# Optimization experiments

Hardware: AMD Instinct MI355X
Metric: run time of the kernel (lower is better)

The kernel has to match this reference:

```python
import jax, jax.numpy as jnp
import numpy as np

N, E, D, H = 100000, 1250000, 64, 128
EPS = 1e-5


def sage_bn_relu(x, src, dst, W_self, b_self, W_neigh, gamma, beta):
    # mean aggregation over in-neighbors (DGL SAGEConv 'mean')
    n = x.shape[0]
    deg = jax.ops.segment_sum(jnp.ones((src.shape[0],), x.dtype), dst, num_segments=n)
    agg = jax.ops.segment_sum(x[src], dst, num_segments=n)  # [N, d]
    neigh = agg / jnp.maximum(deg, 1.0)[:, None]             # zero in-degree -> 0
    h = x @ W_self + b_self + neigh @ W_neigh                # fc_self + fc_neigh
    # BatchNorm1d (training-mode batch statistics, biased variance)
    mu = h.mean(0)
    var = jnp.mean((h - mu) ** 2, axis=0)
    h = (h - mu) * jax.lax.rsqrt(var + EPS) * gamma + beta
    return jax.nn.relu(h)  # dropout omitted (deterministic eval)


def setup_inputs() -> dict:
    key = jax.random.key(0)
    ks = jax.random.split(key, 32)
    inp = {
        "x": jax.random.normal(ks[0], (N, D), jnp.float32),
        "src": jax.random.randint(ks[1], (E,), 0, N),
        "dst": jax.random.randint(ks[2], (E,), 0, N),
    }
    dims = [(D, H), (H, H), (H, H)]
    k = 3
    for i, (din, dout) in enumerate(dims):
        s = 1.0 / np.sqrt(din)
        inp[f"W_self{i}"] = jax.random.uniform(ks[k], (din, dout), jnp.float32, -s, s); k += 1
        inp[f"b_self{i}"] = jnp.zeros((dout,), jnp.float32)
        inp[f"W_neigh{i}"] = jax.random.uniform(ks[k], (din, dout), jnp.float32, -s, s); k += 1
        inp[f"gamma{i}"] = jnp.ones((dout,), jnp.float32)
        inp[f"beta{i}"] = jnp.zeros((dout,), jnp.float32)
    s = 1.0 / np.sqrt(H)
    inp["Wc"] = jax.random.uniform(ks[k], (H, 2), jnp.float32, -s, s)
    inp["bc"] = jnp.zeros((2,), jnp.float32)
    return inp


def reference(x, src, dst,
              W_self0, b_self0, W_neigh0, gamma0, beta0,
              W_self1, b_self1, W_neigh1, gamma1, beta1,
              W_self2, b_self2, W_neigh2, gamma2, beta2,
              Wc, bc):
    h = sage_bn_relu(x, src, dst, W_self0, b_self0, W_neigh0, gamma0, beta0)
    h = sage_bn_relu(h, src, dst, W_self1, b_self1, W_neigh1, gamma1, beta1)
    h = sage_bn_relu(h, src, dst, W_self2, b_self2, W_neigh2, gamma2, beta2)
    return h @ Wc + bc  # [N, 2]
```

## Files before the change

kernel.cpp:

```cpp
#include <hip/hip_runtime.h>


#define N_NODES 100000
#define N_EDGES 1250000
#define NB 1563
#define BSZ 64
#define CAP 1024
#define BPART 256
#define NREP 8
#define INVN (1.0f / 100000.0f)

typedef short bf16x8 __attribute__((ext_vector_type(8)));
typedef float f32x4 __attribute__((ext_vector_type(4)));
typedef unsigned short u16x8 __attribute__((ext_vector_type(8)));
typedef unsigned short u16x4 __attribute__((ext_vector_type(4)));
typedef unsigned short u16x2 __attribute__((ext_vector_type(2)));

__device__ __forceinline__ float bf2f(unsigned short u) {
  union { unsigned int i; float f; } c; c.i = ((unsigned int)u) << 16; return c.f;
}
__device__ __forceinline__ unsigned short f2bf(float f) {
  union { float f; unsigned int i; } c; c.f = f;
  unsigned int r = (c.i + 0x7FFFu + ((c.i >> 16) & 1u)) >> 16;
  return (unsigned short)r;
}
__device__ __forceinline__ void bn_st(const float* stats, const float* gam,
                                      const float* bet, int c, float& s, float& t) {
  float sum = 0.f, sq = 0.f;
  #pragma unroll
  for (int r = 0; r < NREP; r++) {
    sum += stats[r * 256 + c];
    sq  += stats[r * 256 + 128 + c];
  }
  float mu = sum * INVN;
  float var = sq * INVN - mu * mu;
  s = gam[c] * rsqrtf(var + 1e-5f);
  t = bet[c] - mu * s;
}
__device__ __forceinline__ void gload_lds16(const void* g, void* l) {
  __builtin_amdgcn_global_load_lds(
      (const __attribute__((address_space(1))) unsigned int*)g,
      (__attribute__((address_space(3))) unsigned int*)l, 16, 0, 0);
}

__global__ __launch_bounds__(256) void k_prep(
    const float* __restrict__ x, unsigned short* __restrict__ x16,
    const float* __restrict__ W0s, const float* __restrict__ W0n,
    const float* __restrict__ W1s, const float* __restrict__ W1n,
    const float* __restrict__ W2s, const float* __restrict__ W2n,
    unsigned short* __restrict__ wt, float* __restrict__ stats3,
    const int* __restrict__ dst, int* __restrict__ hist, int E) {
  __shared__ int hh[NB];
  int blk = blockIdx.x, t = threadIdx.x;
  if (blk < 6250) {
    int i = blk * 256 + t;
    float4 v = ((const float4*)x)[i];
    u16x4 o;
    o.x = f2bf(v.x); o.y = f2bf(v.y); o.z = f2bf(v.z); o.w = f2bf(v.w);
    ((u16x4*)x16)[i] = o;
  } else if (blk < 6570) {
    int i = (blk - 6250) * 256 + t;
    if (i < 16384) {
      const float* W = (i < 8192) ? W0s : W0n;
      unsigned short* o = wt + (i < 8192 ? 0 : 8192);
      int j = i & 8191;
      int c = j >> 6, k = j & 63;
      o[j] = f2bf(W[k * 128 + c]);
    } else {
      int j = i - 16384;
      int sel = j >> 14;
      j &= 16383;
      const float* W = (sel == 0) ? W1s : (sel == 1) ? W1n : (sel == 2) ? W2s : W2n;
      unsigned short* o = wt + 16384 + sel * 16384;
      int c = j >> 7, k = j & 127;
      o[j] = f2bf(W[k * 128 + c]);
    }
  } else if (blk == 6570) {
    for (int i = t; i < 3 * NREP * 256; i += 256) stats3[i] = 0.f;
  } else {
    int hb = blk - 6571;
    int chunk = (E + BPART - 1) / BPART;
    int start = hb * chunk;
    int end = min(E, start + chunk);
    for (int b = t; b < NB; b += 256) hh[b] = 0;
    __syncthreads();
    for (int e = start + t; e < end; e += 256) atomicAdd(&hh[dst[e] >> 6], 1);
    __syncthreads();
    for (int b = t; b < NB; b += 256) hist[hb * NB + b] = hh[b];
  }
}

__global__ __launch_bounds__(256) void k_scan(const int* __restrict__ hist,
                                              int* __restrict__ base,
                                              int* __restrict__ gcursor) {
  int bb = blockIdx.x * 256 + threadIdx.x;
  if (bb >= NB) return;
  int run = 0;
  for (int r0 = 0; r0 < BPART; r0 += 16) {
    int v[16];
    #pragma unroll
    for (int u = 0; u < 16; u++) v[u] = hist[(r0 + u) * NB + bb];
    #pragma unroll
    for (int u = 0; u < 16; u++) { base[(r0 + u) * NB + bb] = run; run += v[u]; }
  }
  gcursor[bb] = run;
}

__global__ __launch_bounds__(256) void k_scatter(const int* __restrict__ src,
                                                 const int* __restrict__ dst,
                                                 const int* __restrict__ base,
                                                 unsigned int* __restrict__ part, int E) {
  __shared__ int cur[NB];
  int t = threadIdx.x;
  int chunk = (E + BPART - 1) / BPART;
  int start = blockIdx.x * chunk;
  int end = min(E, start + chunk);
  for (int b = t; b < NB; b += 256) cur[b] = base[blockIdx.x * NB + b];
  __syncthreads();
  for (int e = start + t; e < end; e += 256) {
    int d = dst[e];
    int b = d >> 6;
    int pos = atomicAdd(&cur[b], 1);
    if ((unsigned)pos < (unsigned)CAP)
      part[(size_t)b * CAP + pos] = (unsigned)src[e] | ((unsigned)(d & 63) << 17);
  }
}

template <int DIN, bool BN>
__global__ __launch_bounds__(512, 8) void k_layer(
    const unsigned short* __restrict__ h, const unsigned short* __restrict__ W1t,
    const unsigned short* __restrict__ W2t, const float* __restrict__ bias,
    const unsigned int* __restrict__ part, const int* __restrict__ gcursor,
    unsigned short* __restrict__ C, float* __restrict__ stats, int M,
    const float* __restrict__ statsP, const float* __restrict__ gamP,
    const float* __restrict__ betP) {
  __shared__ unsigned short neighT[64 * DIN];
  __shared__ unsigned eord[CAP];
  __shared__ unsigned short Bs[2][128 * 32];
  __shared__ int cnt[BSZ], offv[BSZ], cur[BSZ];
  __shared__ int stealCtr;
  __shared__ float sBN[128], tBN[128];
  unsigned* eraw = (unsigned*)neighT;
  float* redS = (float*)eord;
  float* redQ = redS + 512;

  constexpr int SWZM = (DIN == 128) ? 15 : 7;
  constexpr int KS = DIN / 32;
  int t = threadIdx.x;
  int lane = t & 63, w = t >> 6;
  int l15 = lane & 15, quad = lane >> 4;
  int bkt = blockIdx.x;
  int node0 = bkt * BSZ;
  int nn = min(BSZ, M - node0);

  if (t < BSZ) cnt[t] = 0;
  if (t == 0) stealCtr = 0;
  if (BN && t < 128) bn_st(statsP, gamP, betP, t, sBN[t], tBN[t]);
  __syncthreads();

  int ec = gcursor[bkt];
  ec = max(0, min(ec, CAP));
  for (int i = t; i < ec; i += 512) {
    unsigned wd = part[(size_t)bkt * CAP + i];
    eraw[i] = wd;
    atomicAdd(&cnt[wd >> 17], 1);
  }
  __syncthreads();
  if (w == 0) {
    int v = cnt[lane];
    int incl = v;
    #pragma unroll
    for (int o = 1; o < 64; o <<= 1) {
      int u = __shfl_up(incl, o);
      if (lane >= o) incl += u;
    }
    offv[lane] = incl - v;
    cur[lane] = incl - v;
  }
  __syncthreads();
  for (int i = t; i < ec; i += 512) {
    unsigned wd = eraw[i];
    int p = atomicAdd(&cur[wd >> 17], 1);
    eord[p] = wd & 0x1FFFF;
  }
  __syncthreads();

  const int G = DIN / 8;
  int li = t & (G - 1);
  float sreg[8], treg[8];
  if (BN) {
    #pragma unroll
    for (int k = 0; k < 8; k++) { sreg[k] = sBN[li * 8 + k]; treg[k] = tBN[li * 8 + k]; }
  }
  for (;;) {
    int nd0 = 0;
    if (li == 0) nd0 = atomicAdd(&stealCtr, 1);
    int nd = __shfl(nd0, 0, G);
    if (nd >= BSZ) break;
    u16x8 o;
    if (nd >= nn) {
      #pragma unroll
      for (int k = 0; k < 8; k++) o[k] = 0;
    } else {
      int s = offv[nd], c = cnt[nd];
      int e = s + c;
      float acc[8] = {0.f, 0.f, 0.f, 0.f, 0.f, 0.f, 0.f, 0.f};
      int j = s;
      for (; j + 2 <= e; j += 2) {
        int sn0 = eord[j], sn1 = eord[j + 1];
        u16x8 v0 = *(const u16x8*)&h[(size_t)sn0 * DIN + li * 8];
        u16x8 v1 = *(const u16x8*)&h[(size_t)sn1 * DIN + li * 8];
        if (BN) {
          #pragma unroll
          for (int k = 0; k < 8; k++)
            acc[k] += fmaxf(fmaf(bf2f(v0[k]), sreg[k], treg[k]), 0.f)
                    + fmaxf(fmaf(bf2f(v1[k]), sreg[k], treg[k]), 0.f);
        } else {
          #pragma unroll
          for (int k = 0; k < 8; k++) acc[k] += bf2f(v0[k]) + bf2f(v1[k]);
        }
      }
      if (j < e) {
        int sn = eord[j];
        u16x8 v = *(const u16x8*)&h[(size_t)sn * DIN + li * 8];
        if (BN) {
          #pragma unroll
          for (int k = 0; k < 8; k++)
            acc[k] += fmaxf(fmaf(bf2f(v[k]), sreg[k], treg[k]), 0.f);
        } else {
          #pragma unroll
          for (int k = 0; k < 8; k++) acc[k] += bf2f(v[k]);
        }
      }
      float inv = 1.0f / fmaxf((float)c, 1.0f);
      #pragma unroll
      for (int k = 0; k < 8; k++) o[k] = f2bf(acc[k] * inv);
    }
    *(u16x8*)&neighT[nd * DIN + ((li * 8) ^ ((nd & SWZM) << 3))] = o;
  }

  const int strip = w >> 1;
  const int ch = w & 1;
  const int row = strip * 16 + l15;
  f32x4 acc4[4];
  #pragma unroll
  for (int ct = 0; ct < 4; ct++) acc4[ct] = (f32x4){0.f, 0.f, 0.f, 0.f};

  auto stageBs = [&](int s, int bi) {
    const unsigned short* Wt = (s < KS) ? W1t : W2t;
    int k0 = ((s < KS) ? s : s - KS) * 32;
    int r = t >> 2, prt = t & 3;
    gload_lds16(&Wt[(size_t)r * DIN + k0 + prt * 8], &Bs[bi][(w * 64) * 8]);
  };
  stageBs(0, 0);
  __syncthreads();

  int cb = 0;
  #pragma unroll
  for (int s = 0; s < 2 * KS; s++) {
    if (s + 1 < 2 * KS) stageBs(s + 1, cb ^ 1);
    bf16x8 af;
    if (s < KS) {
      int k0 = s * 32;
      u16x8 v = *(const u16x8*)&h[(size_t)(node0 + row) * DIN + k0 + quad * 8];
      if (BN) {
        #pragma unroll
        for (int j = 0; j < 8; j++) {
          int c = k0 + quad * 8 + j;
          v[j] = f2bf(fmaxf(fmaf(bf2f(v[j]), sBN[c], tBN[c]), 0.f));
        }
      }
      af = *(bf16x8*)&v;
    } else {
      int cc = (s - KS) * 32 + quad * 8;
      u16x8 v = *(const u16x8*)&neighT[row * DIN + (cc ^ ((row & SWZM) << 3))];
      af = *(bf16x8*)&v;
    }
    #pragma unroll
    for (int ct = 0; ct < 4; ct++) {
      bf16x8 bfr = *(const bf16x8*)&Bs[cb][(ch * 64 + ct * 16 + l15) * 32 + quad * 8];
      acc4[ct] = __builtin_amdgcn_mfma_f32_16x16x32_bf16(af, bfr, acc4[ct], 0, 0, 0);
    }
    if (s + 1 < 2 * KS) __syncthreads();
    cb ^= 1;
  }

  float bcol[4], ls[4], lq[4];
  #pragma unroll
  for (int ct = 0; ct < 4; ct++) {
    bcol[ct] = bias[ch * 64 + ct * 16 + l15];
    ls[ct] = 0.f; lq[ct] = 0.f;
  }
  #pragma unroll
  for (int r = 0; r < 4; r++) {
    int orow = node0 + strip * 16 + quad * 4 + r;
    if (orow < M) {
      #pragma unroll
      for (int ct = 0; ct < 4; ct++) {
        float v = acc4[ct][r] + bcol[ct];
        C[(size_t)orow * 128 + ch * 64 + ct * 16 + l15] = f2bf(v);
        ls[ct] += v; lq[ct] += v * v;
      }
    }
  }
  #pragma unroll
  for (int ct = 0; ct < 4; ct++) {
    ls[ct] += __shfl_xor(ls[ct], 16); ls[ct] += __shfl_xor(ls[ct], 32);
    lq[ct] += __shfl_xor(lq[ct], 16); lq[ct] += __shfl_xor(lq[ct], 32);
  }
  if (quad == 0) {
    #pragma unroll
    for (int ct = 0; ct < 4; ct++) {
      redS[w * 64 + ct * 16 + l15] = ls[ct];
      redQ[w * 64 + ct * 16 + l15] = lq[ct];
    }
  }
  __syncthreads();
  if (t < 128) {
    int ch2 = t >> 6, c6 = t & 63;
    float s = 0.f, q = 0.f;
    #pragma unroll
    for (int st = 0; st < 4; st++) {
      s += redS[(st * 2 + ch2) * 64 + c6];
      q += redQ[(st * 2 + ch2) * 64 + c6];
    }
    int rep = (bkt & (NREP - 1)) * 256;
    atomicAdd(&stats[rep + t], s);
    atomicAdd(&stats[rep + 128 + t], q);
  }
}

__global__ __launch_bounds__(256) void k_final(
    const unsigned short* __restrict__ h,
    const float* __restrict__ statsP, const float* __restrict__ gamP,
    const float* __restrict__ betP, const float* __restrict__ Wc,
    const float* __restrict__ bc, float* __restrict__ out, int n) {
  __shared__ float sS[128], sT[128];
  int t = threadIdx.x;
  if (t < 128) bn_st(statsP, gamP, betP, t, sS[t], sT[t]);
  __syncthreads();
  int lane = t & 63;
  int row = blockIdx.x * 4 + (t >> 6);
  if (row >= n) return;
  int c0 = lane * 2;
  u16x2 hv = *(const u16x2*)&h[(size_t)row * 128 + c0];
  float4 w4 = ((const float4*)Wc)[lane];
  float v0 = fmaxf(fmaf(bf2f(hv.x), sS[c0], sT[c0]), 0.f);
  float v1 = fmaxf(fmaf(bf2f(hv.y), sS[c0 + 1], sT[c0 + 1]), 0.f);
  float acc0 = v0 * w4.x + v1 * w4.z;
  float acc1 = v0 * w4.y + v1 * w4.w;
  #pragma unroll
  for (int off = 32; off > 0; off >>= 1) {
    acc0 += __shfl_down(acc0, off);
    acc1 += __shfl_down(acc1, off);
  }
  if (lane == 0) {
    out[row * 2 + 0] = acc0 + bc[0];
    out[row * 2 + 1] = acc1 + bc[1];
  }
}

extern "C" void kernel_launch(void* const* d_in, const int* in_sizes, int n_in,
                              void* d_out, int out_size, void* d_ws, size_t ws_size,
                              hipStream_t stream) {
  const float* x   = (const float*)d_in[0];
  const int* src   = (const int*)d_in[1];
  const int* dst   = (const int*)d_in[2];
  const float* Wself[3] = {(const float*)d_in[3], (const float*)d_in[8],  (const float*)d_in[13]};
  const float* bself[3] = {(const float*)d_in[4], (const float*)d_in[9],  (const float*)d_in[14]};
  const float* Wngh[3]  = {(const float*)d_in[5], (const float*)d_in[10], (const float*)d_in[15]};
  const float* gam[3]   = {(const float*)d_in[6], (const float*)d_in[11], (const float*)d_in[16]};
  const float* bet[3]   = {(const float*)d_in[7], (const float*)d_in[12], (const float*)d_in[17]};
  const float* Wc = (const float*)d_in[18];
  const float* bc = (const float*)d_in[19];
  float* out = (float*)d_out;

  const int N = N_NODES, E = N_EDGES;

  unsigned short* x16 = (unsigned short*)d_ws;
  unsigned short* b0  = x16 + (size_t)N * 64;
  unsigned short* b1  = b0 + (size_t)N * 128;
  unsigned short* b2  = b1 + (size_t)N * 128;
  unsigned short* wt  = b2 + (size_t)N * 128;
  unsigned int* part  = (unsigned int*)(wt + 81920);
  int* gcursor  = (int*)(part + (size_t)NB * CAP);
  float* stats3 = (float*)(gcursor + NB);

  int* hist = (int*)b1;
  int* base = hist + (size_t)BPART * NB;

  k_prep<<<6571 + BPART, 256, 0, stream>>>(
      x, x16, Wself[0], Wngh[0], Wself[1], Wngh[1], Wself[2], Wngh[2],
      wt, stats3, dst, hist, E);

  k_scan<<<(NB + 255) / 256, 256, 0, stream>>>(hist, base, gcursor);
  k_scatter<<<BPART, 256, 0, stream>>>(src, dst, base, part, E);

  k_layer<64, false><<<NB, 512, 0, stream>>>(
      x16, wt + 0, wt + 8192, bself[0], part, gcursor, b1, stats3 + 0, N,
      nullptr, nullptr, nullptr);
  k_layer<128, true><<<NB, 512, 0, stream>>>(
      b1, wt + 16384, wt + 32768, bself[1], part, gcursor, b2, stats3 + 2048, N,
      stats3 + 0, gam[0], bet[0]);
  k_layer<128, true><<<NB, 512, 0, stream>>>(
      b2, wt + 49152, wt + 65536, bself[2], part, gcursor, b1, stats3 + 4096, N,
      stats3 + 2048, gam[1], bet[1]);

  k_final<<<(N + 3) / 4, 256, 0, stream>>>(b1, stats3 + 4096, gam[2], bet[2],
                                           Wc, bc, out, N);
}
```

Measured before the change: 357.5 us.

## Fuse edge histogram, scan and scatter into one atomic-reservation partition kernel

The three-kernel bucketing (per-block histogram, column scan, scatter) is replaced by one kernel. Each block builds an LDS histogram, reserves space per bucket with a global atomicAdd on a padded cursor array, then scatters its edges. This removes two kernel launches and the hist/base round trip through global memory, at the cost of non-deterministic edge order within a bucket. It also doubles the BN stat replicas to reduce atomic contention and has k_final process four rows per wave.

Result: faster. 334.3 us (median of 2 runs) (-6.5%).

```diff
diff --git a/kernel.cpp b/kernel.cpp
--- a/kernel.cpp
+++ b/kernel.cpp
@@ -7,7 +7,8 @@
 #define BSZ 64
 #define CAP 1024
 #define BPART 256
-#define NREP 8
+#define NREP 16
+#define GSTRIDE 16
 #define INVN (1.0f / 100000.0f)
 
 typedef short bf16x8 __attribute__((ext_vector_type(8)));
@@ -49,8 +50,7 @@
     const float* __restrict__ W1s, const float* __restrict__ W1n,
     const float* __restrict__ W2s, const float* __restrict__ W2n,
     unsigned short* __restrict__ wt, float* __restrict__ stats3,
-    const int* __restrict__ dst, int* __restrict__ hist, int E) {
-  __shared__ int hh[NB];
+    int* __restrict__ gcursor) {
   int blk = blockIdx.x, t = threadIdx.x;
   if (blk < 6250) {
     int i = blk * 256 + t;
@@ -75,52 +75,36 @@
       int c = j >> 7, k = j & 127;
       o[j] = f2bf(W[k * 128 + c]);
     }
-  } else if (blk == 6570) {
+  } else {
     for (int i = t; i < 3 * NREP * 256; i += 256) stats3[i] = 0.f;
-  } else {
-    int hb = blk - 6571;
-    int chunk = (E + BPART - 1) / BPART;
-    int start = hb * chunk;
-    int end = min(E, start + chunk);
-    for (int b = t; b < NB; b += 256) hh[b] = 0;
-    __syncthreads();
-    for (int e = start + t; e < end; e += 256) atomicAdd(&hh[dst[e] >> 6], 1);
-    __syncthreads();
-    for (int b = t; b < NB; b += 256) hist[hb * NB + b] = hh[b];
-  }
-}
-
-__global__ __launch_bounds__(256) void k_scan(const int* __restrict__ hist,
-                                              int* __restrict__ base,
-                                              int* __restrict__ gcursor) {
-  int bb = blockIdx.x * 256 + threadIdx.x;
-  if (bb >= NB) return;
-  int run = 0;
-  for (int r0 = 0; r0 < BPART; r0 += 16) {
-    int v[16];
-    #pragma unroll
-    for (int u = 0; u < 16; u++) v[u] = hist[(r0 + u) * NB + bb];
-    #pragma unroll
-    for (int u = 0; u < 16; u++) { base[(r0 + u) * NB + bb] = run; run += v[u]; }
-  }
-  gcursor[bb] = run;
-}
-
-__global__ __launch_bounds__(256) void k_scatter(const int* __restrict__ src,
-                                                 const int* __restrict__ dst,
-                                                 const int* __restrict__ base,
-                                                 unsigned int* __restrict__ part, int E) {
-  __shared__ int cur[NB];
+    for (int i = t; i < NB * GSTRIDE; i += 256) gcursor[i] = 0;
+  }
+}
+
+__global__ __launch_bounds__(512) void k_part(const int* __restrict__ src,
+                                              const int* __restrict__ dst,
+                                              int* __restrict__ gcursor,
+                                              unsigned int* __restrict__ part, int E) {
+  __shared__ int hh[NB];
+  __shared__ int bbase[NB];
   int t = threadIdx.x;
   int chunk = (E + BPART - 1) / BPART;
   int start = blockIdx.x * chunk;
   int end = min(E, start + chunk);
-  for (int b = t; b < NB; b += 256) cur[b] = base[blockIdx.x * NB + b];
-  __syncthreads();
-  for (int e = start + t; e < end; e += 256) {
+  for (int b = t; b < NB; b += 512) hh[b] = 0;
+  __syncthreads();
+  for (int e = start + t; e < end; e += 512) atomicAdd(&hh[dst[e] >> 6], 1);
+  __syncthreads();
+  for (int b = t; b < NB; b += 512) {
+    int c = hh[b];
+    bbase[b] = c ? atomicAdd(&gcursor[b * GSTRIDE], c) : 0;
+    hh[b] = 0;
+  }
+  __syncthreads();
+  for (int e = start + t; e < end; e += 512) {
     int d = dst[e];
     int b = d >> 6;
-    int pos = atomicAdd(&cur[b], 1);
+    int pos = bbase[b] + atomicAdd(&hh[b], 1);
     if ((unsigned)pos < (unsigned)CAP)
       part[(size_t)b * CAP + pos] = (unsigned)src[e] | ((unsigned)(d & 63) << 17);
   }
@@ -158,7 +142,7 @@
   if (BN && t < 128) bn_st(statsP, gamP, betP, t, sBN[t], tBN[t]);
   __syncthreads();
 
-  int ec = gcursor[bkt];
+  int ec = gcursor[bkt * GSTRIDE];
   ec = max(0, min(ec, CAP));
   for (int i = t; i < ec; i += 512) {
     unsigned wd = part[(size_t)bkt * CAP + i];
@@ -340,23 +324,28 @@
   if (t < 128) bn_st(statsP, gamP, betP, t, sS[t], sT[t]);
   __syncthreads();
   int lane = t & 63;
-  int row = blockIdx.x * 4 + (t >> 6);
-  if (row >= n) return;
+  int wv = t >> 6;
   int c0 = lane * 2;
-  u16x2 hv = *(const u16x2*)&h[(size_t)row * 128 + c0];
+  float s0 = sS[c0], t0 = sT[c0], s1 = sS[c0 + 1], t1 = sT[c0 + 1];
   float4 w4 = ((const float4*)Wc)[lane];
-  float v0 = fmaxf(fmaf(bf2f(hv.x), sS[c0], sT[c0]), 0.f);
-  float v1 = fmaxf(fmaf(bf2f(hv.y), sS[c0 + 1], sT[c0 + 1]), 0.f);
-  float acc0 = v0 * w4.x + v1 * w4.z;
-  float acc1 = v0 * w4.y + v1 * w4.w;
-  #pragma unroll
-  for (int off = 32; off > 0; off >>= 1) {
-    acc0 += __shfl_down(acc0, off);
-    acc1 += __shfl_down(acc1, off);
-  }
-  if (lane == 0) {
-    out[row * 2 + 0] = acc0 + bc[0];
-    out[row * 2 + 1] = acc1 + bc[1];
+  #pragma unroll
+  for (int r = 0; r < 4; r++) {
+    int row = blockIdx.x * 16 + wv * 4 + r;
+    if (row >= n) break;
+    u16x2 hv = *(const u16x2*)&h[(size_t)row * 128 + c0];
+    float v0 = fmaxf(fmaf(bf2f(hv.x), s0, t0), 0.f);
+    float v1 = fmaxf(fmaf(bf2f(hv.y), s1, t1), 0.f);
+    float acc0 = v0 * w4.x + v1 * w4.z;
+    float acc1 = v0 * w4.y + v1 * w4.w;
+    #pragma unroll
+    for (int off = 32; off > 0; off >>= 1) {
+      acc0 += __shfl_down(acc0, off);
+      acc1 += __shfl_down(acc1, off);
+    }
+    if (lane == 0) {
+      out[row * 2 + 0] = acc0 + bc[0];
+      out[row * 2 + 1] = acc1 + bc[1];
+    }
   }
 }
 
@@ -384,28 +373,24 @@
   unsigned short* wt  = b2 + (size_t)N * 128;
   unsigned int* part  = (unsigned int*)(wt + 81920);
   int* gcursor  = (int*)(part + (size_t)NB * CAP);
-  float* stats3 = (float*)(gcursor + NB);
-
-  int* hist = (int*)b1;
-  int* base = hist + (size_t)BPART * NB;
-
-  k_prep<<<6571 + BPART, 256, 0, stream>>>(
+  float* stats3 = (float*)(gcursor + NB * GSTRIDE);
+
+  k_prep<<<6571, 256, 0, stream>>>(
       x, x16, Wself[0], Wngh[0], Wself[1], Wngh[1], Wself[2], Wngh[2],
-      wt, stats3, dst, hist, E);
-
-  k_scan<<<(NB + 255) / 256, 256, 0, stream>>>(hist, base, gcursor);
-  k_scatter<<<BPART, 256, 0, stream>>>(src, dst, base, part, E);
+      wt, stats3, gcursor);
+
+  k_part<<<BPART, 512, 0, stream>>>(src, dst, gcursor, part, E);
 
   k_layer<64, false><<<NB, 512, 0, stream>>>(
       x16, wt + 0, wt + 8192, bself[0], part, gcursor, b1, stats3 + 0, N,
       nullptr, nullptr, nullptr);
   k_layer<128, true><<<NB, 512, 0, stream>>>(
-      b1, wt + 16384, wt + 32768, bself[1], part, gcursor, b2, stats3 + 2048, N,
+      b1, wt + 16384, wt + 32768, bself[1], part, gcursor, b2, stats3 + 4096, N,
       stats3 + 0, gam[0], bet[0]);
   k_layer<128, true><<<NB, 512, 0, stream>>>(
-      b2, wt + 49152, wt + 65536, bself[2], part, gcursor, b1, stats3 + 4096, N,
-      stats3 + 2048, gam[1], bet[1]);
-
-  k_final<<<(N + 3) / 4, 256, 0, stream>>>(b1, stats3 + 4096, gam[2], bet[2],
-                                           Wc, bc, out, N);
-}
+      b2, wt + 49152, wt + 65536, bself[2], part, gcursor, b1, stats3 + 8192, N,
+      stats3 + 4096, gam[1], bet[1]);
+
+  k_final<<<(N + 15) / 16, 256, 0, stream>>>(b1, stats3 + 8192, gam[2], bet[2],
+                                             Wc, bc, out, N);
+}
```
